# Performance work log

Measured on AMD Instinct MI355X. Metric: run time of the kernel, lower is better.

Reference implementation:

```python
import math
import jax, jax.numpy as jnp
import numpy as np

B, H, W, C = 16, 64, 64, 192
WS, SHIFT, NH = 16, 8, 6
D = C // NH
N = WS * WS
HID = 4 * C
EPS = 1e-5


def _static_tables():
    # relative position index (N, N)
    coords = np.stack(np.meshgrid(np.arange(WS), np.arange(WS), indexing='ij'))  # (2, WS, WS)
    cf = coords.reshape(2, -1)
    rel = (cf[:, :, None] - cf[:, None, :]).transpose(1, 2, 0)  # (N, N, 2)
    rel[:, :, 0] += WS - 1
    rel[:, :, 1] += WS - 1
    rel[:, :, 0] *= 2 * WS - 1
    rel_idx = rel.sum(-1)  # (N, N)
    # log-spaced continuous relative coords table ((2WS-1)^2, 2)
    r = np.arange(-(WS - 1), WS, dtype=np.float32)
    tab = np.stack(np.meshgrid(r, r, indexing='ij'), axis=-1)  # (2WS-1, 2WS-1, 2)
    tab = tab / (WS - 1) * 8.0
    tab = np.sign(tab) * np.log2(np.abs(tab) + 1.0) / np.log2(8.0)
    # shifted-window attention mask (nW, N, N)
    img = np.zeros((H, W))
    cnt = 0
    for hs in (slice(0, -WS), slice(-WS, -SHIFT), slice(-SHIFT, None)):
        for ws_ in (slice(0, -WS), slice(-WS, -SHIFT), slice(-SHIFT, None)):
            img[hs, ws_] = cnt
            cnt += 1
    win = img.reshape(H // WS, WS, W // WS, WS).transpose(0, 2, 1, 3).reshape(-1, N)
    diff = win[:, None, :] - win[:, :, None]
    mask = np.where(diff != 0, -100.0, 0.0).astype(np.float32)
    return jnp.asarray(rel_idx), jnp.asarray(tab.reshape(-1, 2)), jnp.asarray(mask)

REL_IDX, CPB_TABLE, ATTN_MASK = _static_tables()


def setup_inputs() -> dict:
    key = jax.random.key(0)
    ks = jax.random.split(key, 24)
    s = 0.02
    return {
        'hidden_states': jax.random.normal(ks[0], (B, H * W, C), jnp.float32),
        'time': jax.random.uniform(ks[1], (B,), jnp.float32),
        'q_w': jax.random.normal(ks[2], (C, C), jnp.float32) * s,
        'q_b': jnp.zeros((C,), jnp.float32),
        'k_w': jax.random.normal(ks[3], (C, C), jnp.float32) * s,
        'v_w': jax.random.normal(ks[4], (C, C), jnp.float32) * s,
        'v_b': jnp.zeros((C,), jnp.float32),
        'logit_scale': jnp.full((NH, 1, 1), math.log(10.0), jnp.float32),
        'cpb_w1': jax.random.normal(ks[5], (512, 2), jnp.float32) * s,
        'cpb_b1': jnp.zeros((512,), jnp.float32),
        'cpb_w2': jax.random.normal(ks[6], (NH, 512), jnp.float32) * s,
        'proj_w': jax.random.normal(ks[7], (C, C), jnp.float32) * s,
        'proj_b': jnp.zeros((C,), jnp.float32),
        'ln1_ww': jax.random.normal(ks[8], (C, 1), jnp.float32) * s,
        'ln1_wb': jnp.ones((C,), jnp.float32),
        'ln1_bw': jax.random.normal(ks[9], (C, 1), jnp.float32) * s,
        'ln1_bb': jnp.zeros((C,), jnp.float32),
        'fc1_w': jax.random.normal(ks[10], (HID, C), jnp.float32) * s,
        'fc1_b': jnp.zeros((HID,), jnp.float32),
        'fc2_w': jax.random.normal(ks[11], (C, HID), jnp.float32) * s,
        'fc2_b': jnp.zeros((C,), jnp.float32),
        'ln2_ww': jax.random.normal(ks[12], (C, 1), jnp.float32) * s,
        'ln2_wb': jnp.ones((C,), jnp.float32),
        'ln2_bw': jax.random.normal(ks[13], (C, 1), jnp.float32) * s,
        'ln2_bb': jnp.zeros((C,), jnp.float32),
    }


def _cond_ln(x, time, ww, wb, bw, bb):
    mean = x.mean(-1, keepdims=True)
    var = (x ** 2).mean(-1, keepdims=True) - mean ** 2
    xn = (x - mean) / jnp.sqrt(var + EPS)
    t = time.reshape(-1, 1)
    w = (t @ ww.T + wb)[:, None, :]
    b = (t @ bw.T + bb)[:, None, :]
    return w * xn + b


def _forward(hidden_states, time, q_w, q_b, k_w, v_w, v_b, logit_scale,
             cpb_w1, cpb_b1, cpb_w2, proj_w, proj_b,
             ln1_ww, ln1_wb, ln1_bw, ln1_bb,
             fc1_w, fc1_b, fc2_w, fc2_b,
             ln2_ww, ln2_wb, ln2_bw, ln2_bb):
    nWh, nWw = H // WS, W // WS
    nW = nWh * nWw
    x = hidden_states.reshape(B, H, W, C)
    x = jnp.roll(x, (-SHIFT, -SHIFT), axis=(1, 2))
    # window partition -> (B*nW, N, C)
    xw = x.reshape(B, nWh, WS, nWw, WS, C).transpose(0, 1, 3, 2, 4, 5).reshape(-1, N, C)
    q = (xw @ q_w.T + q_b).reshape(-1, N, NH, D).transpose(0, 2, 1, 3)
    k = (xw @ k_w.T).reshape(-1, N, NH, D).transpose(0, 2, 1, 3)
    v = (xw @ v_w.T + v_b).reshape(-1, N, NH, D).transpose(0, 2, 1, 3)
    # cosine attention with learned temperature
    qn = q / jnp.linalg.norm(q, axis=-1, keepdims=True)
    kn = k / jnp.linalg.norm(k, axis=-1, keepdims=True)
    scale = jnp.exp(jnp.minimum(logit_scale, math.log(100.0)))  # (NH,1,1)
    attn = jnp.einsum('whnd,whmd->whnm', qn, kn) * scale
    # continuous relative position bias
    tbl = jnp.maximum(CPB_TABLE @ cpb_w1.T + cpb_b1, 0.0) @ cpb_w2.T  # (M, NH)
    rpb = tbl[REL_IDX.reshape(-1)].reshape(N, N, NH).transpose(2, 0, 1)
    attn = attn + 16.0 * jax.nn.sigmoid(rpb)[None]
    # shifted-window mask
    attn = attn.reshape(B, nW, NH, N, N) + ATTN_MASK[None, :, None]
    attn = jax.nn.softmax(attn.reshape(-1, NH, N, N), axis=-1)
    out = jnp.einsum('whnm,whmd->whnd', attn, v).transpose(0, 2, 1, 3).reshape(-1, N, C)
    out = out @ proj_w.T + proj_b
    # window reverse + un-roll
    out = out.reshape(B, nWh, nWw, WS, WS, C).transpose(0, 1, 3, 2, 4, 5).reshape(B, H, W, C)
    out = jnp.roll(out, (SHIFT, SHIFT), axis=(1, 2)).reshape(B, H * W, C)
    # res-post-norm residual blocks
    h = hidden_states + _cond_ln(out, time, ln1_ww, ln1_wb, ln1_bw, ln1_bb)
    mlp = jax.nn.gelu(h @ fc1_w.T + fc1_b, approximate=False) @ fc2_w.T + fc2_b
    return h + _cond_ln(mlp, time, ln2_ww, ln2_wb, ln2_bw, ln2_bb)


def reference(hidden_states, time, q_w, q_b, k_w, v_w, v_b, logit_scale,
              cpb_w1, cpb_b1, cpb_w2, proj_w, proj_b,
              ln1_ww, ln1_wb, ln1_bw, ln1_bb,
              fc1_w, fc1_b, fc2_w, fc2_b,
              ln2_ww, ln2_wb, ln2_bw, ln2_bb):
    return _forward(hidden_states, time, q_w, q_b, k_w, v_w, v_b, logit_scale,
                    cpb_w1, cpb_b1, cpb_w2, proj_w, proj_b,
                    ln1_ww, ln1_wb, ln1_bw, ln1_bb,
                    fc1_w, fc1_b, fc2_w, fc2_b,
                    ln2_ww, ln2_wb, ln2_bw, ln2_bb)
```

## Files before the change

kernel.cpp:

```cpp
#include <hip/hip_runtime.h>
#include <hip/hip_bf16.h>
#include <hip/hip_fp16.h>
#include <math.h>

#define BB 16
#define CC 192
#define SHIFT 8
#define NH 6
#define DD 32
#define NN 256
#define HID 768
#define NWIN 256
#define NROWS 65536

#define OFF_TBL   0ll
#define OFF_BIASM (32ll<<10)
#define OFF_WQKV  (3200ll<<10)
#define OFF_PWB   (3424ll<<10)
#define OFF_W1B   (3500ll<<10)
#define OFF_W2B   (3800ll<<10)
#define OFF_BQKV  (4096ll<<10)
#define OFF_WTAB  (4104ll<<10)
#define OFF_XB    (8ll<<20)
#define OFF_Q     (32ll<<20)
#define OFF_K     (56ll<<20)
#define OFF_V     (80ll<<20)
#define OFF_AO    (104ll<<20)
#define OFF_HB    OFF_XB
#define OFF_H2    OFF_Q

typedef __attribute__((ext_vector_type(4)))  float f32x4;
typedef __attribute__((ext_vector_type(16))) float f32x16;
typedef __attribute__((ext_vector_type(8)))  short bf16x8;

__device__ __forceinline__ void gload16(const void* g, void* l) {
    __builtin_amdgcn_global_load_lds(
        (const __attribute__((address_space(1))) void*)g,
        (__attribute__((address_space(3))) void*)l, 16, 0, 0);
}

__device__ __forceinline__ float b2f(short s) {
    unsigned u = ((unsigned)(unsigned short)s) << 16;
    return __builtin_bit_cast(float, u);
}
__device__ __forceinline__ short f2b(float f) {
    return __builtin_bit_cast(short, __float2bfloat16(f));
}
__device__ __forceinline__ unsigned pk2(float lo, float hi) {
    unsigned a = (unsigned short)f2b(lo);
    unsigned b = (unsigned short)f2b(hi);
    return a | (b << 16);
}

__device__ __forceinline__ float gelu_fast(float x) {
    float x2 = x * x;
    float z = x * fmaf(0.0713548353f, x2, 1.5957691216f);
    float e = __expf(-z);
    return x * __builtin_amdgcn_rcpf(1.0f + e);
}

__device__ __forceinline__ float cpb_coord(int u) {
    float t = (float)u * (8.0f / 15.0f);
    return copysignf(log2f(fabsf(t) + 1.0f) * (1.0f / 3.0f), t);
}

__global__ __launch_bounds__(512) void k_tbl(
    const float* __restrict__ w1, const float* __restrict__ b1,
    const float* __restrict__ w2, float* __restrict__ tbl)
{
    __shared__ float r[512];
    int m = blockIdx.x;
    int a = m / 31, b = m % 31;
    float c0 = cpb_coord(a - 15);
    float c1 = cpb_coord(b - 15);
    int hd = threadIdx.x;
    float rv = c0 * w1[hd * 2 + 0] + c1 * w1[hd * 2 + 1] + b1[hd];
    r[hd] = fmaxf(rv, 0.0f);
    __syncthreads();
    if (hd < NH) {
        float s = 0.0f;
        for (int k = 0; k < 512; ++k) s += r[k] * w2[hd * 512 + k];
        tbl[m * NH + hd] = s;
    }
}

__global__ __launch_bounds__(256) void k_biasm(
    const float* __restrict__ tbl, __half* __restrict__ biasp)
{
    int bid = blockIdx.x;
    int ty = bid / (NH * NN);
    int rem = bid % (NH * NN);
    int h = rem >> 8, i = rem & 255;
    int j = threadIdx.x;
    int yi = i >> 4, xi = i & 15, yj = j >> 4, xj = j & 15;
    int idx = (yi - yj + 15) * 31 + (xi - xj + 15);
    float v = 16.0f / (1.0f + __expf(-tbl[idx * NH + h]));
    int rhi = (ty & 2) ? ((yi < SHIFT) ? 1 : 2) : 0;
    int rwi = (ty & 1) ? ((xi < SHIFT) ? 1 : 2) : 0;
    int rhj = (ty & 2) ? ((yj < SHIFT) ? 1 : 2) : 0;
    int rwj = (ty & 1) ? ((xj < SHIFT) ? 1 : 2) : 0;
    if (rhi * 3 + rwi != rhj * 3 + rwj) v -= 100.0f;
    int jc = j & 31;
    int r = (jc & 3) + 4 * (jc >> 3);
    int g = (jc >> 2) & 1;
    int pos = (j & ~31) + g * 16 + r;
    biasp[(((size_t)ty * NH + h) * NN + i) * NN + pos] = __float2half(v);
}

__global__ __launch_bounds__(256) void k_cvt(
    const float* __restrict__ qw, const float* __restrict__ kw,
    const float* __restrict__ vw, const float* __restrict__ pw,
    const float* __restrict__ fc1w, const float* __restrict__ fc2w,
    const float* __restrict__ q_b, const float* __restrict__ v_b,
    __hip_bfloat16* __restrict__ wqkv, __hip_bfloat16* __restrict__ pwb,
    __hip_bfloat16* __restrict__ w1b, __hip_bfloat16* __restrict__ w2b,
    float* __restrict__ bqkv)
{
    int i = blockIdx.x * 256 + threadIdx.x;
    const int S1 = 36864, S2 = 73728, S3 = 110592, S4 = 147456,
              S5 = 294912, S6 = 442368, S7 = 442944;
    if (i < S3) {
        const float* src = (i < S1) ? qw : (i < S2) ? kw : vw;
        int off = (i < S1) ? i : (i < S2) ? i - S1 : i - S2;
        wqkv[i] = __float2bfloat16(src[off]);
    } else if (i < S4) { pwb[i - S3] = __float2bfloat16(pw[i - S3]); }
    else if (i < S5)   { w1b[i - S4] = __float2bfloat16(fc1w[i - S4]); }
    else if (i < S6)   { w2b[i - S5] = __float2bfloat16(fc2w[i - S5]); }
    else if (i < S7) {
        int j = i - S6;
        bqkv[j] = (j < 192) ? q_b[j] : (j < 384) ? 0.0f : v_b[j - 384];
    }
}

__global__ __launch_bounds__(256) void k_wtab(
    const float* __restrict__ time,
    const float* __restrict__ w1w, const float* __restrict__ w1b_,
    const float* __restrict__ b1w, const float* __restrict__ b1b_,
    const float* __restrict__ w2w, const float* __restrict__ w2b_,
    const float* __restrict__ b2w, const float* __restrict__ b2b_,
    float* __restrict__ wtab)
{
    int idx = blockIdx.x * 256 + threadIdx.x;
    int t = idx / 3072, rem = idx % 3072;
    int b = rem / 192, c = rem % 192;
    float tm = time[b];
    float v;
    if (t == 0)      v = tm * w1w[c] + w1b_[c];
    else if (t == 1) v = tm * b1w[c] + b1b_[c];
    else if (t == 2) v = tm * w2w[c] + w2b_[c];
    else             v = tm * b2w[c] + b2b_[c];
    wtab[idx] = v;
}

__global__ __launch_bounds__(256) void k_gather(
    const float* __restrict__ x, __hip_bfloat16* __restrict__ xb)
{
    int idx = blockIdx.x * 256 + threadIdx.x;
    int r = idx / 48, c4 = idx % 48;
    int win = r >> 8, n = r & 255;
    int b = win >> 4, wh = (win >> 2) & 3, ww = win & 3;
    int yi = n >> 4, xi = n & 15;
    int sy = (wh * 16 + yi + SHIFT) & 63;
    int sx = (ww * 16 + xi + SHIFT) & 63;
    float4 v = *(const float4*)&x[((size_t)b * 4096 + sy * 64 + sx) * CC + c4 * 4];
    union { short h[4]; short4 s4; } u;
    u.h[0] = f2b(v.x); u.h[1] = f2b(v.y); u.h[2] = f2b(v.z); u.h[3] = f2b(v.w);
    *(short4*)&((short*)xb)[(size_t)r * CC + c4 * 4] = u.s4;
}

#define STAGE_SWZ(dstLds, srcPtr, ldK, nR)                                  \
    for (int r_ = 0; r_ < (nR); ++r_) {                                     \
        int off_ = r_ * 256 + tid;                                          \
        int row_ = off_ >> 3, cb_ = off_ & 7;                               \
        int ce_ = ((cb_ ^ (row_ & 7)) << 3);                                \
        gload16((srcPtr) + (size_t)row_ * (ldK) + ce_, &(dstLds)[off_ * 8]); \
    }

__global__ __launch_bounds__(256) void k_qkvgemm(
    const __hip_bfloat16* __restrict__ A, const __hip_bfloat16* __restrict__ Bw,
    const float* __restrict__ bias, const float* __restrict__ lscale,
    __hip_bfloat16* __restrict__ qbo, __hip_bfloat16* __restrict__ kbo,
    __hip_bfloat16* __restrict__ vbo)
{
    __shared__ short lds[12288];
    short* As = lds;
    short* Bs = lds + 8192;
    int tid = threadIdx.x, lane = tid & 63;
    int w = tid >> 6, wr = w >> 1, wc = w & 1;
    int bm = blockIdx.x, bn = blockIdx.y;

    f32x4 acc[4][2];
    #pragma unroll
    for (int fm = 0; fm < 4; ++fm)
        #pragma unroll
        for (int fn = 0; fn < 2; ++fn) acc[fm][fn] = (f32x4)0.0f;

    for (int kt = 0; kt < CC; kt += 64) {
        STAGE_SWZ(As, A + (size_t)(bm * 128) * CC + kt, CC, 4)
        STAGE_SWZ(Bs, Bw + (size_t)(bn * 64) * CC + kt, CC, 2)
        __syncthreads();
        #pragma unroll
        for (int kk = 0; kk < 2; ++kk) {
            int kcq = kk * 4 + (lane >> 4);
            bf16x8 af[4], bfr[2];
            #pragma unroll
            for (int fm = 0; fm < 4; ++fm) {
                int row = wr * 64 + fm * 16 + (lane & 15);
                af[fm] = *(const bf16x8*)&As[row * 64 + ((kcq ^ (row & 7)) << 3)];
            }
            #pragma unroll
            for (int fn = 0; fn < 2; ++fn) {
                int row = wc * 32 + fn * 16 + (lane & 15);
                bfr[fn] = *(const bf16x8*)&Bs[row * 64 + ((kcq ^ (row & 7)) << 3)];
            }
            #pragma unroll
            for (int fm = 0; fm < 4; ++fm)
                #pragma unroll
                for (int fn = 0; fn < 2; ++fn)
                    acc[fm][fn] = __builtin_amdgcn_mfma_f32_16x16x32_bf16(
                        af[fm], bfr[fn], acc[fm][fn], 0, 0, 0);
        }
        __syncthreads();
    }

    bool donorm = (bn < 6);
    bool isq = (bn < 3);
    float qscale = __expf(fminf(lscale[(bn % 3) * 2 + wc], 4.6051702f));
    int bcol = bn * 64 + wc * 32 + (lane & 15);
    #pragma unroll
    for (int fm = 0; fm < 4; ++fm)
        #pragma unroll
        for (int r = 0; r < 4; ++r) {
            float v0 = acc[fm][0][r] + bias[bcol];
            float v1 = acc[fm][1][r] + bias[bcol + 16];
            if (donorm) {
                float s2 = v0 * v0 + v1 * v1;
                s2 += __shfl_xor(s2, 1);
                s2 += __shfl_xor(s2, 2);
                s2 += __shfl_xor(s2, 4);
                s2 += __shfl_xor(s2, 8);
                float rn = rsqrtf(s2);
                if (isq) rn *= qscale;
                v0 *= rn; v1 *= rn;
            }
            int rowl = wr * 64 + fm * 16 + ((lane >> 4) << 2) + r;
            int c0 = wc * 32 + (lane & 15);
            int sw = (rowl & 3) << 4;
            lds[rowl * 64 + (c0 ^ sw)] = f2b(v0);
            lds[rowl * 64 + ((c0 + 16) ^ sw)] = f2b(v1);
        }
    __syncthreads();
    __hip_bfloat16* dst = (bn < 3) ? qbo : (bn < 6) ? kbo : vbo;
    int cb0 = (bn % 3) * 64;
    #pragma unroll
    for (int rr = 0; rr < 2; ++rr) {
        int row = rr * 64 + (tid >> 2);
        int cl = (tid & 3) * 16;
        int cp = cl ^ ((row & 3) << 4);
        bf16x8 a = *(const bf16x8*)&lds[row * 64 + cp];
        bf16x8 b = *(const bf16x8*)&lds[row * 64 + cp + 8];
        size_t base = (size_t)(bm * 128 + row) * CC + cb0 + cl;
        *(bf16x8*)&dst[base] = a;
        *(bf16x8*)&dst[base + 8] = b;
    }
}

#define VTP 260
__global__ __launch_bounds__(256, 2) void k_attn(
    const __hip_bfloat16* __restrict__ qb,
    const __hip_bfloat16* __restrict__ kb,
    const __hip_bfloat16* __restrict__ vb,
    const __half* __restrict__ biasp,
    const float* __restrict__ lscale,
    __hip_bfloat16* __restrict__ ao)
{
    __shared__ short Vt[32 * VTP];
    int blk = blockIdx.x;
    int win = blk / NH, h = blk % NH;
    int wwh = (win >> 2) & 3, www = win & 3;
    int ty = (((wwh == 3) ? 2 : 0) | ((www == 3) ? 1 : 0));
    int tid = threadIdx.x;
    int wv = tid >> 6, lane = tid & 63;
    int c = lane & 31, g = lane >> 5;

    float scale = __expf(fminf(lscale[h], 4.6051702f));
    float M = scale + 16.0f;

    {
        int j = wv * 64 + lane;
        const short* vsrc = (const short*)vb + ((size_t)(win * NN + j)) * CC + h * DD;
        #pragma unroll
        for (int q4 = 0; q4 < 4; ++q4) {
            bf16x8 t = *(const bf16x8*)(vsrc + q4 * 8);
            #pragma unroll
            for (int e = 0; e < 8; ++e)
                Vt[(q4 * 8 + e) * VTP + j] = t[e];
        }
    }
    __syncthreads();

    const short* qsrc = (const short*)qb + ((size_t)(win * NN + wv * 64)) * CC + h * DD;
    bf16x8 qf[2][2];
    #pragma unroll
    for (int fq = 0; fq < 2; ++fq)
        #pragma unroll
        for (int kd = 0; kd < 2; ++kd)
            qf[fq][kd] = *(const bf16x8*)(qsrc + (size_t)(32 * fq + c) * CC + 16 * kd + 8 * g);

    f32x16 acc_o[2];
    acc_o[0] = (f32x16)0.0f; acc_o[1] = (f32x16)0.0f;
    float lsum[2] = {0.0f, 0.0f};

    const short* kbase = (const short*)kb + ((size_t)(win * NN)) * CC + h * DD;
    const __half* bbase = biasp + (((size_t)ty * NH + h) * NN) * NN;

    for (int t = 0; t < 4; ++t) {
        int jt = t * 64;
        bf16x8 kf[2][2];
        #pragma unroll
        for (int fj = 0; fj < 2; ++fj)
            #pragma unroll
            for (int kd = 0; kd < 2; ++kd)
                kf[fj][kd] = *(const bf16x8*)(kbase + (size_t)(jt + 32 * fj + c) * CC + 16 * kd + 8 * g);
        f32x16 st[2][2];
        #pragma unroll
        for (int fj = 0; fj < 2; ++fj)
            #pragma unroll
            for (int fq = 0; fq < 2; ++fq) {
                f32x16 tmp = __builtin_amdgcn_mfma_f32_32x32x16_bf16(
                    kf[fj][0], qf[fq][0], (f32x16)0.0f, 0, 0, 0);
                st[fj][fq] = __builtin_amdgcn_mfma_f32_32x32x16_bf16(
                    kf[fj][1], qf[fq][1], tmp, 0, 0, 0);
            }
        #pragma unroll
        for (int fj = 0; fj < 2; ++fj) {
            bf16x8 vfr[2];
            #pragma unroll
            for (int rb = 0; rb < 2; ++rb) {
                int j0 = jt + 32 * fj + 16 * rb + 4 * g;
                uint2 va = *(const uint2*)&Vt[c * VTP + j0];
                uint2 vb2 = *(const uint2*)&Vt[c * VTP + j0 + 8];
                union { unsigned u[4]; bf16x8 v; } vu;
                vu.u[0] = va.x; vu.u[1] = va.y; vu.u[2] = vb2.x; vu.u[3] = vb2.y;
                vfr[rb] = vu.v;
            }
            #pragma unroll
            for (int fq = 0; fq < 2; ++fq) {
                const __half* bp = bbase + (size_t)(wv * 64 + 32 * fq + c) * NN
                                   + jt + 32 * fj + g * 16;
                union { uint4 u; __half2 h2[4]; } ba, bbu;
                ba.u  = *(const uint4*)bp;
                bbu.u = *(const uint4*)(bp + 8);
                float p[16];
                #pragma unroll
                for (int q4 = 0; q4 < 4; ++q4) {
                    float2 fa = __half22float2(ba.h2[q4]);
                    p[2 * q4 + 0] = st[fj][fq][2 * q4 + 0] + fa.x;
                    p[2 * q4 + 1] = st[fj][fq][2 * q4 + 1] + fa.y;
                    float2 fb = __half22float2(bbu.h2[q4]);
                    p[8 + 2 * q4 + 0] = st[fj][fq][8 + 2 * q4 + 0] + fb.x;
                    p[8 + 2 * q4 + 1] = st[fj][fq][8 + 2 * q4 + 1] + fb.y;
                }
                #pragma unroll
                for (int r = 0; r < 16; ++r) p[r] = __expf(p[r] - M);
                #pragma unroll
                for (int r = 0; r < 16; ++r) lsum[fq] += p[r];
                #pragma unroll
                for (int rb = 0; rb < 2; ++rb) {
                    union { unsigned u[4]; bf16x8 v; } pu;
                    pu.u[0] = pk2(p[8 * rb + 0], p[8 * rb + 1]);
                    pu.u[1] = pk2(p[8 * rb + 2], p[8 * rb + 3]);
                    pu.u[2] = pk2(p[8 * rb + 4], p[8 * rb + 5]);
                    pu.u[3] = pk2(p[8 * rb + 6], p[8 * rb + 7]);
                    acc_o[fq] = __builtin_amdgcn_mfma_f32_32x32x16_bf16(
                        pu.v, vfr[rb], acc_o[fq], 0, 0, 0);
                }
            }
        }
    }

    #pragma unroll
    for (int fq = 0; fq < 2; ++fq) {
        lsum[fq] += __shfl_xor(lsum[fq], 32);
        float rlv = 1.0f / lsum[fq];
        #pragma unroll
        for (int r = 0; r < 16; ++r) {
            int rho = (r & 3) + 8 * (r >> 2) + 4 * g;
            float rli = __shfl(rlv, rho);
            int row = wv * 64 + 32 * fq + rho;
            ao[((size_t)(win * NN + row)) * CC + h * DD + c] =
                __float2bfloat16(acc_o[fq][r] * rli);
        }
    }
}

__global__ __launch_bounds__(256) void k_projgemm(
    const __hip_bfloat16* __restrict__ ao,
    const __hip_bfloat16* __restrict__ pwb,
    const float* __restrict__ pbias,
    const float* __restrict__ wtab,
    __hip_bfloat16* xbhb)
{
    __shared__ short lds[16384];
    __shared__ float part[64][4];
    short* As = lds;
    short* Bs = lds + 4096;
    int tid = threadIdx.x, lane = tid & 63;
    int w = tid >> 6, wr = w >> 1, wc = w & 1;
    int bm = blockIdx.x;

    f32x4 acc[2][6];
    #pragma unroll
    for (int fm = 0; fm < 2; ++fm)
        #pragma unroll
        for (int fn = 0; fn < 6; ++fn) acc[fm][fn] = (f32x4)0.0f;

    for (int kt = 0; kt < CC; kt += 64) {
        STAGE_SWZ(As, ao + (size_t)(bm * 64) * CC + kt, CC, 2)
        STAGE_SWZ(Bs, pwb + kt, CC, 6)
        __syncthreads();
        #pragma unroll
        for (int kk = 0; kk < 2; ++kk) {
            int kcq = kk * 4 + (lane >> 4);
            bf16x8 af[2], bfr[6];
            #pragma unroll
            for (int fm = 0; fm < 2; ++fm) {
                int row = wr * 32 + fm * 16 + (lane & 15);
                af[fm] = *(const bf16x8*)&As[row * 64 + ((kcq ^ (row & 7)) << 3)];
            }
            #pragma unroll
            for (int fn = 0; fn < 6; ++fn) {
                int row = wc * 96 + fn * 16 + (lane & 15);
                bfr[fn] = *(const bf16x8*)&Bs[row * 64 + ((kcq ^ (row & 7)) << 3)];
            }
            #pragma unroll
            for (int fm = 0; fm < 2; ++fm)
                #pragma unroll
                for (int fn = 0; fn < 6; ++fn)
                    acc[fm][fn] = __builtin_amdgcn_mfma_f32_16x16x32_bf16(
                        af[fm], bfr[fn], acc[fm][fn], 0, 0, 0);
        }
        __syncthreads();
    }

    #pragma unroll
    for (int fm = 0; fm < 2; ++fm)
        #pragma unroll
        for (int r = 0; r < 4; ++r) {
            int rowl = wr * 32 + fm * 16 + ((lane >> 4) << 2) + r;
            float s = 0.0f, s2 = 0.0f;
            #pragma unroll
            for (int fn = 0; fn < 6; ++fn) {
                int col = wc * 96 + fn * 16 + (lane & 15);
                float v = acc[fm][fn][r] + pbias[col];
                lds[rowl * 200 + col] = f2b(v);
                s += v; s2 += v * v;
            }
            #pragma unroll
            for (int m = 1; m < 16; m <<= 1) {
                s  += __shfl_xor(s, m);
                s2 += __shfl_xor(s2, m);
            }
            if ((lane & 15) == 0) {
                part[rowl][wc * 2]     = s;
                part[rowl][wc * 2 + 1] = s2;
            }
        }
    __syncthreads();

    int row = tid >> 2;
    int cb = (tid & 3) * 48;
    float s  = part[row][0] + part[row][2];
    float s2 = part[row][1] + part[row][3];
    float mean = s * (1.0f / 192.0f);
    float rstd = rsqrtf(s2 * (1.0f / 192.0f) - mean * mean + 1e-5f);
    int rw = bm * 64 + row;
    const float* wt = wtab + (rw >> 12) * 192;
    const float* bt = wtab + 16 * 192 + (rw >> 12) * 192;
    #pragma unroll
    for (int c8 = 0; c8 < 6; ++c8) {
        int c = cb + c8 * 8;
        bf16x8 lv = *(const bf16x8*)&lds[row * 200 + c];
        bf16x8 xv = *(const bf16x8*)&xbhb[(size_t)rw * CC + c];
        float4 w0 = *(const float4*)&wt[c], w1 = *(const float4*)&wt[c + 4];
        float4 b0 = *(const float4*)&bt[c], b1 = *(const float4*)&bt[c + 4];
        float wv[8] = {w0.x, w0.y, w0.z, w0.w, w1.x, w1.y, w1.z, w1.w};
        float bv[8] = {b0.x, b0.y, b0.z, b0.w, b1.x, b1.y, b1.z, b1.w};
        bf16x8 o;
        #pragma unroll
        for (int e = 0; e < 8; ++e) {
            float xn = (b2f(lv[e]) - mean) * rstd;
            o[e] = f2b(b2f(xv[e]) + wv[e] * xn + bv[e]);
        }
        *(bf16x8*)&xbhb[(size_t)rw * CC + c] = o;
    }
}

__global__ __launch_bounds__(256) void k_fc1(
    const __hip_bfloat16* __restrict__ A, const __hip_bfloat16* __restrict__ Bw,
    const float* __restrict__ bias, __hip_bfloat16* __restrict__ Cout)
{
    __shared__ short lds[16384];
    short* As = lds;
    short* Bs = lds + 8192;
    int tid = threadIdx.x;
    int lane = tid & 63;
    int w = tid >> 6, wr = w >> 1, wc = w & 1;
    int bm = blockIdx.x, bn = blockIdx.y;

    f32x4 acc[4][4];
    #pragma unroll
    for (int fm = 0; fm < 4; ++fm)
        #pragma unroll
        for (int fn = 0; fn < 4; ++fn)
            acc[fm][fn] = (f32x4)0.0f;

    for (int kt = 0; kt < CC; kt += 64) {
        STAGE_SWZ(As, A + (size_t)(bm * 128) * CC + kt, CC, 4)
        STAGE_SWZ(Bs, Bw + (size_t)(bn * 128) * CC + kt, CC, 4)
        __syncthreads();
        #pragma unroll
        for (int kk = 0; kk < 2; ++kk) {
            int kcq = kk * 4 + (lane >> 4);
            bf16x8 af[4], bfr[4];
            #pragma unroll
            for (int fm = 0; fm < 4; ++fm) {
                int row = wr * 64 + fm * 16 + (lane & 15);
                af[fm] = *(const bf16x8*)&As[row * 64 + ((kcq ^ (row & 7)) << 3)];
            }
            #pragma unroll
            for (int fn = 0; fn < 4; ++fn) {
                int row = wc * 64 + fn * 16 + (lane & 15);
                bfr[fn] = *(const bf16x8*)&Bs[row * 64 + ((kcq ^ (row & 7)) << 3)];
            }
            #pragma unroll
            for (int fm = 0; fm < 4; ++fm)
                #pragma unroll
                for (int fn = 0; fn < 4; ++fn)
                    acc[fm][fn] = __builtin_amdgcn_mfma_f32_16x16x32_bf16(
                        af[fm], bfr[fn], acc[fm][fn], 0, 0, 0);
        }
        __syncthreads();
    }

    #pragma unroll
    for (int fm = 0; fm < 4; ++fm)
        #pragma unroll
        for (int fn = 0; fn < 4; ++fn) {
            int coll = wc * 64 + fn * 16 + (lane & 15);
            float bv = bias[bn * 128 + coll];
            #pragma unroll
            for (int r = 0; r < 4; ++r) {
                int rowl = wr * 64 + fm * 16 + ((lane >> 4) << 2) + r;
                float v = gelu_fast(acc[fm][fn][r] + bv);
                lds[rowl * 128 + (coll ^ ((rowl & 7) << 4))] = f2b(v);
            }
        }
    __syncthreads();
    #pragma unroll
    for (int rr = 0; rr < 4; ++rr) {
        int row = rr * 32 + (tid >> 3);
        int cl = (tid & 7) * 16;
        int cp = cl ^ ((row & 7) << 4);
        bf16x8 a = *(const bf16x8*)&lds[row * 128 + cp];
        bf16x8 b = *(const bf16x8*)&lds[row * 128 + cp + 8];
        size_t base = (size_t)(bm * 128 + row) * HID + bn * 128 + cl;
        *(bf16x8*)&Cout[base] = a;
        *(bf16x8*)&Cout[base + 8] = b;
    }
}

__global__ __launch_bounds__(256) void k_fc2ln(
    const __hip_bfloat16* __restrict__ A,
    const __hip_bfloat16* __restrict__ Bw,
    const float* __restrict__ bias,
    const __hip_bfloat16* __restrict__ hb,
    const float* __restrict__ wtab,
    float* __restrict__ out)
{
    __shared__ short lds[16384];
    __shared__ float part[64][4];
    short* As = lds;
    short* Bs = lds + 4096;
    int tid = threadIdx.x, lane = tid & 63;
    int w = tid >> 6, wr = w >> 1, wc = w & 1;
    int bm = blockIdx.x;

    f32x4 acc[2][6];
    #pragma unroll
    for (int fm = 0; fm < 2; ++fm)
        #pragma unroll
        for (int fn = 0; fn < 6; ++fn) acc[fm][fn] = (f32x4)0.0f;

    for (int kt = 0; kt < HID; kt += 64) {
        STAGE_SWZ(As, A + (size_t)(bm * 64) * HID + kt, HID, 2)
        STAGE_SWZ(Bs, Bw + kt, HID, 6)
        __syncthreads();
        #pragma unroll
        for (int kk = 0; kk < 2; ++kk) {
            int kcq = kk * 4 + (lane >> 4);
            bf16x8 af[2], bfr[6];
            #pragma unroll
            for (int fm = 0; fm < 2; ++fm) {
                int row = wr * 32 + fm * 16 + (lane & 15);
                af[fm] = *(const bf16x8*)&As[row * 64 + ((kcq ^ (row & 7)) << 3)];
            }
            #pragma unroll
            for (int fn = 0; fn < 6; ++fn) {
                int row = wc * 96 + fn * 16 + (lane & 15);
                bfr[fn] = *(const bf16x8*)&Bs[row * 64 + ((kcq ^ (row & 7)) << 3)];
            }
            #pragma unroll
            for (int fm = 0; fm < 2; ++fm)
                #pragma unroll
                for (int fn = 0; fn < 6; ++fn)
                    acc[fm][fn] = __builtin_amdgcn_mfma_f32_16x16x32_bf16(
                        af[fm], bfr[fn], acc[fm][fn], 0, 0, 0);
        }
        __syncthreads();
    }

    #pragma unroll
    for (int fm = 0; fm < 2; ++fm)
        #pragma unroll
        for (int r = 0; r < 4; ++r) {
            int rowl = wr * 32 + fm * 16 + ((lane >> 4) << 2) + r;
            float s = 0.0f, s2 = 0.0f;
            #pragma unroll
            for (int fn = 0; fn < 6; ++fn) {
                int col = wc * 96 + fn * 16 + (lane & 15);
                float v = acc[fm][fn][r] + bias[col];
                lds[rowl * 200 + col] = f2b(v);
                s += v; s2 += v * v;
            }
            #pragma unroll
            for (int m = 1; m < 16; m <<= 1) {
                s  += __shfl_xor(s, m);
                s2 += __shfl_xor(s2, m);
            }
            if ((lane & 15) == 0) {
                part[rowl][wc * 2]     = s;
                part[rowl][wc * 2 + 1] = s2;
            }
        }
    __syncthreads();

    int row = tid >> 2;
    int cb = (tid & 3) * 48;
    float s  = part[row][0] + part[row][2];
    float s2 = part[row][1] + part[row][3];
    float mean = s * (1.0f / 192.0f);
    float rstd = rsqrtf(s2 * (1.0f / 192.0f) - mean * mean + 1e-5f);
    int rw = bm * 64 + row;
    int win = rw >> 8, n = rw & 255, b = rw >> 12;
    int wh = (win >> 2) & 3, wwn = win & 3;
    int y  = (wh * 16 + (n >> 4) + SHIFT) & 63;
    int xq = (wwn * 16 + (n & 15) + SHIFT) & 63;
    size_t rimg = (size_t)b * 4096 + y * 64 + xq;
    const float* wt = wtab + 2 * 16 * 192 + b * 192;
    const float* bt = wtab + 3 * 16 * 192 + b * 192;
    #pragma unroll
    for (int c8 = 0; c8 < 6; ++c8) {
        int c = cb + c8 * 8;
        bf16x8 lv = *(const bf16x8*)&lds[row * 200 + c];
        bf16x8 hv = *(const bf16x8*)&hb[(size_t)rw * CC + c];
        float4 w0 = *(const float4*)&wt[c], w1 = *(const float4*)&wt[c + 4];
        float4 b0 = *(const float4*)&bt[c], b1 = *(const float4*)&bt[c + 4];
        float wv[8] = {w0.x, w0.y, w0.z, w0.w, w1.x, w1.y, w1.z, w1.w};
        float bv[8] = {b0.x, b0.y, b0.z, b0.w, b1.x, b1.y, b1.z, b1.w};
        float4 o0, o1;
        float oo[8];
        #pragma unroll
        for (int e = 0; e < 8; ++e) {
            float xn = (b2f(lv[e]) - mean) * rstd;
            oo[e] = b2f(hv[e]) + wv[e] * xn + bv[e];
        }
        o0.x = oo[0]; o0.y = oo[1]; o0.z = oo[2]; o0.w = oo[3];
        o1.x = oo[4]; o1.y = oo[5]; o1.z = oo[6]; o1.w = oo[7];
        *(float4*)&out[rimg * CC + c] = o0;
        *(float4*)&out[rimg * CC + c + 4] = o1;
    }
}

extern "C" void kernel_launch(void* const* d_in, const int* in_sizes, int n_in,
                              void* d_out, int out_size, void* d_ws, size_t ws_size,
                              hipStream_t stream)
{
    const float* x        = (const float*)d_in[0];
    const float* time     = (const float*)d_in[1];
    const float* q_w      = (const float*)d_in[2];
    const float* q_b      = (const float*)d_in[3];
    const float* k_w      = (const float*)d_in[4];
    const float* v_w      = (const float*)d_in[5];
    const float* v_b      = (const float*)d_in[6];
    const float* lscale   = (const float*)d_in[7];
    const float* cpb_w1   = (const float*)d_in[8];
    const float* cpb_b1   = (const float*)d_in[9];
    const float* cpb_w2   = (const float*)d_in[10];
    const float* proj_w   = (const float*)d_in[11];
    const float* proj_b   = (const float*)d_in[12];
    const float* ln1_ww   = (const float*)d_in[13];
    const float* ln1_wb   = (const float*)d_in[14];
    const float* ln1_bw   = (const float*)d_in[15];
    const float* ln1_bb   = (const float*)d_in[16];
    const float* fc1_w    = (const float*)d_in[17];
    const float* fc1_b    = (const float*)d_in[18];
    const float* fc2_w    = (const float*)d_in[19];
    const float* fc2_b    = (const float*)d_in[20];
    const float* ln2_ww   = (const float*)d_in[21];
    const float* ln2_wb   = (const float*)d_in[22];
    const float* ln2_bw   = (const float*)d_in[23];
    const float* ln2_bb   = (const float*)d_in[24];

    char* ws = (char*)d_ws;
    float* tbl            = (float*)(ws + OFF_TBL);
    __half* biasp         = (__half*)(ws + OFF_BIASM);
    __hip_bfloat16* wqkv  = (__hip_bfloat16*)(ws + OFF_WQKV);
    __hip_bfloat16* pwb   = (__hip_bfloat16*)(ws + OFF_PWB);
    __hip_bfloat16* w1b   = (__hip_bfloat16*)(ws + OFF_W1B);
    __hip_bfloat16* w2b   = (__hip_bfloat16*)(ws + OFF_W2B);
    float* bqkv           = (float*)(ws + OFF_BQKV);
    float* wtab           = (float*)(ws + OFF_WTAB);
    __hip_bfloat16* xb    = (__hip_bfloat16*)(ws + OFF_XB);
    __hip_bfloat16* qb    = (__hip_bfloat16*)(ws + OFF_Q);
    __hip_bfloat16* kb    = (__hip_bfloat16*)(ws + OFF_K);
    __hip_bfloat16* vb    = (__hip_bfloat16*)(ws + OFF_V);
    __hip_bfloat16* ao    = (__hip_bfloat16*)(ws + OFF_AO);
    __hip_bfloat16* hb    = (__hip_bfloat16*)(ws + OFF_HB);
    __hip_bfloat16* h2    = (__hip_bfloat16*)(ws + OFF_H2);
    float* out            = (float*)d_out;

    k_tbl   <<<961, 512, 0, stream>>>(cpb_w1, cpb_b1, cpb_w2, tbl);
    k_biasm <<<4 * NH * NN, 256, 0, stream>>>(tbl, biasp);
    k_cvt   <<<1731, 256, 0, stream>>>(q_w, k_w, v_w, proj_w, fc1_w, fc2_w,
                                       q_b, v_b, wqkv, pwb, w1b, w2b, bqkv);
    k_wtab  <<<48, 256, 0, stream>>>(time, ln1_ww, ln1_wb, ln1_bw, ln1_bb,
                                     ln2_ww, ln2_wb, ln2_bw, ln2_bb, wtab);
    k_gather<<<12288, 256, 0, stream>>>(x, xb);
    k_qkvgemm<<<dim3(NROWS / 128, 9), 256, 0, stream>>>(xb, wqkv, bqkv, lscale, qb, kb, vb);
    k_attn  <<<NWIN * NH, 256, 0, stream>>>(qb, kb, vb, biasp, lscale, ao);
    k_projgemm<<<NROWS / 64, 256, 0, stream>>>(ao, pwb, proj_b, wtab, xb);
    k_fc1   <<<dim3(NROWS / 128, HID / 128), 256, 0, stream>>>(hb, w1b, fc1_b, h2);
    k_fc2ln <<<NROWS / 64, 256, 0, stream>>>(h2, w2b, fc2_b, hb, wtab, out);
}
```

Baseline: 256.2 us.

## Fold softmax offset and log2e into bias and Q scale, use exp2 in attention

The fixed softmax max offset (scale+16) and the log2(e) factor are moved out of the attention inner loop. The offset is subtracted in the precomputed fp16 bias table and log2(e) is applied both there and in the q normalization scale, so the attention kernel calls a raw exp2 with no subtract or multiply. The attention loop is also restructured to load K per 32-row chunk and interleave QK and PV MFMAs with s_setprio, and launch bounds are raised to 3 blocks per CU to improve occupancy. Storing the offset bias in fp16 loses some precision near -100 masked values, and the occupancy hint may cause register spills.

```diff
diff --git a/kernel.cpp b/kernel.cpp
--- a/kernel.cpp
+++ b/kernel.cpp
@@ -52,6 +52,14 @@
     return a | (b << 16);
 }
 
+__device__ __forceinline__ float fexp2(float x) {
+#if __has_builtin(__builtin_amdgcn_exp2f)
+    return __builtin_amdgcn_exp2f(x);
+#else
+    return __expf(x * 0.69314718056f);
+#endif
+}
+
 __device__ __forceinline__ float gelu_fast(float x) {
     float x2 = x * x;
     float z = x * fmaf(0.0713548353f, x2, 1.5957691216f);
@@ -85,7 +93,8 @@
 }
 
 __global__ __launch_bounds__(256) void k_biasm(
-    const float* __restrict__ tbl, __half* __restrict__ biasp)
+    const float* __restrict__ tbl, const float* __restrict__ lscale,
+    __half* __restrict__ biasp)
 {
     int bid = blockIdx.x;
     int ty = bid / (NH * NN);
@@ -100,6 +109,8 @@
     int rhj = (ty & 2) ? ((yj < SHIFT) ? 1 : 2) : 0;
     int rwj = (ty & 1) ? ((xj < SHIFT) ? 1 : 2) : 0;
     if (rhi * 3 + rwi != rhj * 3 + rwj) v -= 100.0f;
+    float scale = __expf(fminf(lscale[h], 4.6051702f));
+    v = (v - 16.0f - scale) * 1.44269504f;
     int jc = j & 31;
     int r = (jc & 3) + 4 * (jc >> 3);
     int g = (jc >> 2) & 1;
@@ -225,7 +236,7 @@
 
     bool donorm = (bn < 6);
     bool isq = (bn < 3);
-    float qscale = __expf(fminf(lscale[(bn % 3) * 2 + wc], 4.6051702f));
+    float qscale = __expf(fminf(lscale[(bn % 3) * 2 + wc], 4.6051702f)) * 1.44269504f;
     int bcol = bn * 64 + wc * 32 + (lane & 15);
     #pragma unroll
     for (int fm = 0; fm < 4; ++fm)
@@ -266,12 +277,11 @@
 }
 
 #define VTP 260
-__global__ __launch_bounds__(256, 2) void k_attn(
+__global__ __launch_bounds__(256, 3) void k_attn(
     const __hip_bfloat16* __restrict__ qb,
     const __hip_bfloat16* __restrict__ kb,
     const __hip_bfloat16* __restrict__ vb,
     const __half* __restrict__ biasp,
-    const float* __restrict__ lscale,
     __hip_bfloat16* __restrict__ ao)
 {
     __shared__ short Vt[32 * VTP];
@@ -283,9 +293,6 @@
     int wv = tid >> 6, lane = tid & 63;
     int c = lane & 31, g = lane >> 5;
 
-    float scale = __expf(fminf(lscale[h], 4.6051702f));
-    float M = scale + 16.0f;
-
     {
         int j = wv * 64 + lane;
         const short* vsrc = (const short*)vb + ((size_t)(win * NN + j)) * CC + h * DD;
@@ -316,28 +323,28 @@
 
     for (int t = 0; t < 4; ++t) {
         int jt = t * 64;
-        bf16x8 kf[2][2];
-        #pragma unroll
-        for (int fj = 0; fj < 2; ++fj)
-            #pragma unroll
-            for (int kd = 0; kd < 2; ++kd)
-                kf[fj][kd] = *(const bf16x8*)(kbase + (size_t)(jt + 32 * fj + c) * CC + 16 * kd + 8 * g);
-        f32x16 st[2][2];
-        #pragma unroll
-        for (int fj = 0; fj < 2; ++fj)
-            #pragma unroll
-            for (int fq = 0; fq < 2; ++fq) {
-                f32x16 tmp = __builtin_amdgcn_mfma_f32_32x32x16_bf16(
-                    kf[fj][0], qf[fq][0], (f32x16)0.0f, 0, 0, 0);
-                st[fj][fq] = __builtin_amdgcn_mfma_f32_32x32x16_bf16(
-                    kf[fj][1], qf[fq][1], tmp, 0, 0, 0);
-            }
         #pragma unroll
         for (int fj = 0; fj < 2; ++fj) {
+            int jb = jt + 32 * fj;
+            bf16x8 kf0 = *(const bf16x8*)(kbase + (size_t)(jb + c) * CC + 8 * g);
+            bf16x8 kf1 = *(const bf16x8*)(kbase + (size_t)(jb + c) * CC + 16 + 8 * g);
+            f32x16 st[2];
+            __builtin_amdgcn_s_setprio(1);
+            {
+                f32x16 t0 = __builtin_amdgcn_mfma_f32_32x32x16_bf16(
+                    kf0, qf[0][0], (f32x16)0.0f, 0, 0, 0);
+                st[0] = __builtin_amdgcn_mfma_f32_32x32x16_bf16(
+                    kf1, qf[0][1], t0, 0, 0, 0);
+                f32x16 t1 = __builtin_amdgcn_mfma_f32_32x32x16_bf16(
+                    kf0, qf[1][0], (f32x16)0.0f, 0, 0, 0);
+                st[1] = __builtin_amdgcn_mfma_f32_32x32x16_bf16(
+                    kf1, qf[1][1], t1, 0, 0, 0);
+            }
+            __builtin_amdgcn_s_setprio(0);
             bf16x8 vfr[2];
             #pragma unroll
             for (int rb = 0; rb < 2; ++rb) {
-                int j0 = jt + 32 * fj + 16 * rb + 4 * g;
+                int j0 = jb + 16 * rb + 4 * g;
                 uint2 va = *(const uint2*)&Vt[c * VTP + j0];
                 uint2 vb2 = *(const uint2*)&Vt[c * VTP + j0 + 8];
                 union { unsigned u[4]; bf16x8 v; } vu;
@@ -347,7 +354,7 @@
             #pragma unroll
             for (int fq = 0; fq < 2; ++fq) {
                 const __half* bp = bbase + (size_t)(wv * 64 + 32 * fq + c) * NN
-                                   + jt + 32 * fj + g * 16;
+                                   + jb + g * 16;
                 union { uint4 u; __half2 h2[4]; } ba, bbu;
                 ba.u  = *(const uint4*)bp;
                 bbu.u = *(const uint4*)(bp + 8);
@@ -355,26 +362,27 @@
                 #pragma unroll
                 for (int q4 = 0; q4 < 4; ++q4) {
                     float2 fa = __half22float2(ba.h2[q4]);
-                    p[2 * q4 + 0] = st[fj][fq][2 * q4 + 0] + fa.x;
-                    p[2 * q4 + 1] = st[fj][fq][2 * q4 + 1] + fa.y;
+                    p[2 * q4 + 0] = st[fq][2 * q4 + 0] + fa.x;
+                    p[2 * q4 + 1] = st[fq][2 * q4 + 1] + fa.y;
                     float2 fb = __half22float2(bbu.h2[q4]);
-                    p[8 + 2 * q4 + 0] = st[fj][fq][8 + 2 * q4 + 0] + fb.x;
-                    p[8 + 2 * q4 + 1] = st[fj][fq][8 + 2 * q4 + 1] + fb.y;
+                    p[8 + 2 * q4 + 0] = st[fq][8 + 2 * q4 + 0] + fb.x;
+                    p[8 + 2 * q4 + 1] = st[fq][8 + 2 * q4 + 1] + fb.y;
                 }
                 #pragma unroll
-                for (int r = 0; r < 16; ++r) p[r] = __expf(p[r] - M);
+                for (int r = 0; r < 16; ++r) p[r] = fexp2(p[r]);
                 #pragma unroll
                 for (int r = 0; r < 16; ++r) lsum[fq] += p[r];
-                #pragma unroll
-                for (int rb = 0; rb < 2; ++rb) {
-                    union { unsigned u[4]; bf16x8 v; } pu;
-                    pu.u[0] = pk2(p[8 * rb + 0], p[8 * rb + 1]);
-                    pu.u[1] = pk2(p[8 * rb + 2], p[8 * rb + 3]);
-                    pu.u[2] = pk2(p[8 * rb + 4], p[8 * rb + 5]);
-                    pu.u[3] = pk2(p[8 * rb + 6], p[8 * rb + 7]);
-                    acc_o[fq] = __builtin_amdgcn_mfma_f32_32x32x16_bf16(
-                        pu.v, vfr[rb], acc_o[fq], 0, 0, 0);
-                }
+                union { unsigned u[4]; bf16x8 v; } pu0, pu1;
+                pu0.u[0] = pk2(p[0],  p[1]);  pu0.u[1] = pk2(p[2],  p[3]);
+                pu0.u[2] = pk2(p[4],  p[5]);  pu0.u[3] = pk2(p[6],  p[7]);
+                pu1.u[0] = pk2(p[8],  p[9]);  pu1.u[1] = pk2(p[10], p[11]);
+                pu1.u[2] = pk2(p[12], p[13]); pu1.u[3] = pk2(p[14], p[15]);
+                __builtin_amdgcn_s_setprio(1);
+                acc_o[fq] = __builtin_amdgcn_mfma_f32_32x32x16_bf16(
+                    pu0.v, vfr[0], acc_o[fq], 0, 0, 0);
+                acc_o[fq] = __builtin_amdgcn_mfma_f32_32x32x16_bf16(
+                    pu1.v, vfr[1], acc_o[fq], 0, 0, 0);
+                __builtin_amdgcn_s_setprio(0);
             }
         }
     }
@@ -731,14 +739,14 @@
     float* out            = (float*)d_out;
 
     k_tbl   <<<961, 512, 0, stream>>>(cpb_w1, cpb_b1, cpb_w2, tbl);
-    k_biasm <<<4 * NH * NN, 256, 0, stream>>>(tbl, biasp);
+    k_biasm <<<4 * NH * NN, 256, 0, stream>>>(tbl, lscale, biasp);
     k_cvt   <<<1731, 256, 0, stream>>>(q_w, k_w, v_w, proj_w, fc1_w, fc2_w,
                                        q_b, v_b, wqkv, pwb, w1b, w2b, bqkv);
     k_wtab  <<<48, 256, 0, stream>>>(time, ln1_ww, ln1_wb, ln1_bw, ln1_bb,
                                      ln2_ww, ln2_wb, ln2_bw, ln2_bb, wtab);
     k_gather<<<12288, 256, 0, stream>>>(x, xb);
     k_qkvgemm<<<dim3(NROWS / 128, 9), 256, 0, stream>>>(xb, wqkv, bqkv, lscale, qb, kb, vb);
-    k_attn  <<<NWIN * NH, 256, 0, stream>>>(qb, kb, vb, biasp, lscale, ao);
+    k_attn  <<<NWIN * NH, 256, 0, stream>>>(qb, kb, vb, biasp, ao);
     k_projgemm<<<NROWS / 64, 256, 0, stream>>>(ao, pwb, proj_b, wtab, xb);
     k_fc1   <<<dim3(NROWS / 128, HID / 128), 256, 0, stream>>>(hb, w1b, fc1_b, h2);
     k_fc2ln <<<NROWS / 64, 256, 0, stream>>>(h2, w2b, fc2_b, hb, wtab, out);
```

Result: faster. 249.6 us (-2.5%).
